# Kernel tuning notes

Hardware: AMD Instinct MI355X
Metric: run time of the kernel (lower is better)

Reference implementation:

```python
import jax, jax.numpy as jnp
import numpy as np


def causal_conv1d(x, w, b, dilation):
    # x: [B, Cin, S], w: [Cout, Cin, K] -> [B, Cout, S]
    # left pad by dilation*(K-1): equivalent to pad-both-sides + Chomp1d
    pad = dilation * (w.shape[-1] - 1)
    out = jax.lax.conv_general_dilated(
        x, w, window_strides=(1,), padding=[(pad, 0)],
        rhs_dilation=(dilation,), dimension_numbers=('NCH', 'OIH', 'NCH'))
    return out + b[None, :, None]


def temporal_block(x, w1, b1, w2, b2, dilation, ds=None):
    # dropout is identity in eval mode
    out = jax.nn.elu(causal_conv1d(x, w1, b1, dilation))
    out = jax.nn.elu(causal_conv1d(out, w2, b2, dilation))
    if ds is None:
        res = x
    else:
        ds_w, ds_b = ds
        res = causal_conv1d(x, ds_w, ds_b, 1)  # 1x1 downsample conv
    return jax.nn.elu(out + res)


def setup_inputs() -> dict:
    key = jax.random.key(0)
    ks = jax.random.split(key, 12)
    B, Cin, S, C, K, L = 16, 64, 4096, 128, 2, 5
    return {
        'x': jax.random.normal(ks[0], (B, Cin, S), jnp.float32),
        'w1_0': jax.random.normal(ks[1], (C, Cin, K), jnp.float32),
        'b1_0': jax.random.normal(ks[2], (C,), jnp.float32),
        'w2_0': jax.random.normal(ks[3], (C, C, K), jnp.float32),
        'b2_0': jax.random.normal(ks[4], (C,), jnp.float32),
        'ds_w': jax.random.normal(ks[5], (C, Cin, 1), jnp.float32),
        'ds_b': jax.random.normal(ks[6], (C,), jnp.float32),
        'W1': jax.random.normal(ks[7], (L - 1, C, C, K), jnp.float32),
        'B1': jax.random.normal(ks[8], (L - 1, C), jnp.float32),
        'W2': jax.random.normal(ks[9], (L - 1, C, C, K), jnp.float32),
        'B2': jax.random.normal(ks[10], (L - 1, C), jnp.float32),
    }


def reference(x, w1_0, b1_0, w2_0, b2_0, ds_w, ds_b, W1, B1, W2, B2):
    STEP = 3
    num_levels = 1 + W1.shape[0]  # 5
    outputs = [x]
    # layer 0: dilation 1, with downsample (64 -> 128 channels)
    x = temporal_block(x, w1_0, b1_0, w2_0, b2_0, 1, ds=(ds_w, ds_b))
    outputs.append(x)
    # layers 1..L-1: dilation 2**i, no downsample (128 -> 128)
    for i in range(1, num_levels):
        x = temporal_block(x, W1[i - 1], B1[i - 1], W2[i - 1], B2[i - 1], 2 ** i)
        outputs.append(x)
        if i >= STEP and outputs[i - STEP].shape == x.shape:
            x = x + outputs[i - STEP]
    return x
```

## Files before the change

kernel.cpp:

```cpp
#include <hip/hip_runtime.h>
#include <hip/hip_bf16.h>
#include <math.h>


typedef __attribute__((ext_vector_type(8))) short short8;
typedef __attribute__((ext_vector_type(4))) short short4v;
typedef __attribute__((ext_vector_type(4))) float floatx4;

#define S_LEN 4096
#define ROWS 192
#define AREG (ROWS * 128)
#define WBUF (128 * 128)
#define LDS_BYTES ((2 * AREG + 2 * WBUF) * 2)

#define OFF_DS     0
#define OFF_L0C1_0 8192
#define OFF_L0C1_1 16384
#define OFF_L0C2_0 24576
#define OFF_L0C2_1 40960
#define OFF_C1B    57344
#define OFF_C2B    188416

__device__ __forceinline__ float elu_f(float v) {
    return v > 0.0f ? v : (__expf(v) - 1.0f);
}
__device__ __forceinline__ short f2bs(float v) {
    __hip_bfloat16 h = __float2bfloat16(v);
    return *reinterpret_cast<short*>(&h);
}
__device__ __forceinline__ float bs2f(short s) {
    __hip_bfloat16 h = *reinterpret_cast<__hip_bfloat16*>(&s);
    return __bfloat162float(h);
}
__device__ __forceinline__ short4v pack4(const floatx4 v) {
    __hip_bfloat162 p0 = __float22bfloat162_rn(make_float2(v[0], v[1]));
    __hip_bfloat162 p1 = __float22bfloat162_rn(make_float2(v[2], v[3]));
    short4v r;
    r[0] = ((const short*)&p0)[0]; r[1] = ((const short*)&p0)[1];
    r[2] = ((const short*)&p1)[0]; r[3] = ((const short*)&p1)[1];
    return r;
}

__device__ __forceinline__ void gld_lds16(const void* g, void* l) {
    __builtin_amdgcn_global_load_lds(
        (const __attribute__((address_space(1))) void*)g,
        (__attribute__((address_space(3))) void*)l, 16, 0, 0);
}

template<int NSH>
__device__ __forceinline__ void stage_async(short* __restrict__ lds,
                                            const short* __restrict__ src,
                                            int wave, int lane)
{
    constexpr int NI = (NSH * 2) / 16384;
    const char* g = (const char*)src + wave * 1024 + lane * 16;
    char* l = (char*)lds + wave * 1024;
    #pragma unroll
    for (int i = 0; i < NI; ++i)
        gld_lds16(g + i * 16384, l + i * 16384);
}

__device__ __forceinline__ void mkoff(int (&o)[3], int srow, int l16, int quad, int d) {
    #pragma unroll
    for (int nt = 0; nt < 3; ++nt) {
        int r = srow + nt * 16 + l16 - d;
        if (r < 0) r = 0;
        o[nt] = (r >> 4) * 2048 + (r & 15) * 8 + quad * 128;
    }
}

template<int KCH>
__device__ __forceinline__ void conv_tap(const short* __restrict__ Lin,
                                         const short* __restrict__ Lw,
                                         const int (&ao)[3], floatx4 (&acc)[2][3])
{
    short8 wf[2][KCH];
    #pragma unroll
    for (int mt = 0; mt < 2; ++mt)
        #pragma unroll
        for (int kc = 0; kc < KCH; ++kc)
            wf[mt][kc] = *(const short8*)(Lw + mt * (KCH * 512) + kc * 512);
    #pragma unroll
    for (int nt = 0; nt < 3; ++nt) {
        const short* ab = Lin + ao[nt];
        #pragma unroll
        for (int kc = 0; kc < KCH; ++kc) {
            const short8 bf = *(const short8*)(ab + kc * 512);
            #pragma unroll
            for (int mt = 0; mt < 2; ++mt)
                acc[mt][nt] = __builtin_amdgcn_mfma_f32_16x16x32_bf16(wf[mt][kc], bf, acc[mt][nt], 0, 0, 0);
        }
    }
}

__device__ __forceinline__ void zero_acc(floatx4 (&acc)[2][3]) {
    #pragma unroll
    for (int mt = 0; mt < 2; ++mt)
        #pragma unroll
        for (int nt = 0; nt < 3; ++nt) acc[mt][nt] = {0.f, 0.f, 0.f, 0.f};
}

__global__ __launch_bounds__(1024, 4)
void tcn_fused(const float* __restrict__ x,
               const short* __restrict__ wq,
               const float* __restrict__ b1_0, const float* __restrict__ b2_0,
               const float* __restrict__ ds_b, const float* __restrict__ B1,
               const float* __restrict__ B2, float* __restrict__ out)
{
    extern __shared__ short L[];
    short* RA = L;
    short* RB = L + AREG;
    short* W0 = L + 2 * AREG;
    short* W1 = L + 2 * AREG + WBUF;

    const int tid  = threadIdx.x;
    const int wave = tid >> 6, lane = tid & 63;
    const int l16  = lane & 15, quad = lane >> 4;
    const int cobase = (wave & 3) * 32;
    const int srow   = (wave >> 2) * 48;
    const int s0  = blockIdx.x * 128;
    const int s0g = s0 - 64;
    const int b   = blockIdx.y;
    const bool zb = (s0 == 0);

    const int wqb2 = (cobase >> 4) * 1024 + quad * 128 + l16 * 8;
    const int wqb4 = (cobase >> 4) * 2048 + quad * 128 + l16 * 8;
    int aoff0[3], aoffd[3];
    mkoff(aoff0, srow, l16, quad, 0);
    int sb[3];
    #pragma unroll
    for (int nt = 0; nt < 3; ++nt) {
        const int sl = srow + nt * 16 + l16;
        sb[nt] = (sl >> 4) * 2048 + (sl & 15) * 8;
    }
    int ct[2];
    #pragma unroll
    for (int mt = 0; mt < 2; ++mt) {
        const int co4 = cobase + mt * 16 + quad * 4;
        ct[mt] = (co4 >> 5) * 512 + ((co4 >> 3) & 3) * 128 + (co4 & 7);
    }
    bool zr[3];
    #pragma unroll
    for (int nt = 0; nt < 3; ++nt) zr[nt] = zb && (srow + nt * 16 < 64);

    floatx4 acc[2][3];
    short4v x1keep[6];
    short4v dk[6];

    stage_async<8192>(W0, wq + OFF_DS, wave, lane);
    {
        const float* xp = x + (size_t)b * 64 * S_LEN;
        const int ci0 = wave * 4;
        const int cterm = (ci0 >> 5) * 512 + ((ci0 >> 3) & 3) * 128 + (ci0 & 7);
        #pragma unroll
        for (int h = 0; h < 3; ++h) {
            const int r = lane + h * 64;
            const int s = s0g + r;
            short4v pk;
            #pragma unroll
            for (int c4 = 0; c4 < 4; ++c4) {
                const float v = (s >= 0) ? xp[(ci0 + c4) * S_LEN + s] : 0.f;
                pk[c4] = f2bs(v);
            }
            *(short4v*)(RA + (r >> 4) * 2048 + (r & 15) * 8 + cterm) = pk;
        }
    }
    __syncthreads();

    stage_async<8192>(W1, wq + OFF_L0C1_0, wave, lane);
    zero_acc(acc);
    conv_tap<2>(RA, W0 + wqb2, aoff0, acc);
    #pragma unroll
    for (int mt = 0; mt < 2; ++mt) {
        const int co4 = cobase + mt * 16 + quad * 4;
        const floatx4 bb = *(const floatx4*)(ds_b + co4);
        #pragma unroll
        for (int nt = 0; nt < 3; ++nt) {
            floatx4 y = acc[mt][nt] + bb;
            if (zr[nt]) y = {0.f, 0.f, 0.f, 0.f};
            dk[mt * 3 + nt] = pack4(y);
        }
    }
    __syncthreads();

    stage_async<8192>(W0, wq + OFF_L0C1_1, wave, lane);
    mkoff(aoffd, srow, l16, quad, 1);
    zero_acc(acc);
    conv_tap<2>(RA, W1 + wqb2, aoffd, acc);
    __syncthreads();

    stage_async<16384>(W1, wq + OFF_L0C2_0, wave, lane);
    conv_tap<2>(RA, W0 + wqb2, aoff0, acc);
    #pragma unroll
    for (int mt = 0; mt < 2; ++mt) {
        const int co4 = cobase + mt * 16 + quad * 4;
        const floatx4 bb = *(const floatx4*)(b1_0 + co4);
        #pragma unroll
        for (int nt = 0; nt < 3; ++nt) {
            floatx4 y = acc[mt][nt] + bb;
            #pragma unroll
            for (int rr = 0; rr < 4; ++rr) y[rr] = elu_f(y[rr]);
            if (zr[nt]) y = {0.f, 0.f, 0.f, 0.f};
            *(short4v*)(RB + sb[nt] + ct[mt]) = pack4(y);
        }
    }
    __syncthreads();

    stage_async<16384>(W0, wq + OFF_L0C2_1, wave, lane);
    zero_acc(acc);
    conv_tap<4>(RB, W1 + wqb4, aoffd, acc);
    __syncthreads();

    stage_async<16384>(W1, wq + OFF_C1B, wave, lane);
    conv_tap<4>(RB, W0 + wqb4, aoff0, acc);
    #pragma unroll
    for (int mt = 0; mt < 2; ++mt) {
        const int co4 = cobase + mt * 16 + quad * 4;
        const floatx4 bb = *(const floatx4*)(b2_0 + co4);
        #pragma unroll
        for (int nt = 0; nt < 3; ++nt) {
            floatx4 y = acc[mt][nt] + bb;
            const short4v d4 = dk[mt * 3 + nt];
            #pragma unroll
            for (int rr = 0; rr < 4; ++rr) {
                y[rr] = elu_f(y[rr]);
                y[rr] = elu_f(y[rr] + bs2f(d4[rr]));
            }
            if (zr[nt]) y = {0.f, 0.f, 0.f, 0.f};
            const short4v pk = pack4(y);
            *(short4v*)(RA + sb[nt] + ct[mt]) = pk;
            x1keep[mt * 3 + nt] = pk;
        }
    }
    __syncthreads();

    #pragma unroll
    for (int lvl = 0; lvl < 3; ++lvl) {
        const int d = 2 << lvl;
        mkoff(aoffd, srow, l16, quad, d);
        stage_async<16384>(W0, wq + OFF_C1B + lvl * 32768 + 16384, wave, lane);
        zero_acc(acc);
        conv_tap<4>(RA, W1 + wqb4, aoffd, acc);
        __syncthreads();
        stage_async<16384>(W1, wq + OFF_C2B + lvl * 32768, wave, lane);
        conv_tap<4>(RA, W0 + wqb4, aoff0, acc);
        #pragma unroll
        for (int mt = 0; mt < 2; ++mt) {
            const int co4 = cobase + mt * 16 + quad * 4;
            const floatx4 bb = *(const floatx4*)(B1 + lvl * 128 + co4);
            #pragma unroll
            for (int nt = 0; nt < 3; ++nt) {
                floatx4 y = acc[mt][nt] + bb;
                #pragma unroll
                for (int rr = 0; rr < 4; ++rr) y[rr] = elu_f(y[rr]);
                if (zr[nt]) y = {0.f, 0.f, 0.f, 0.f};
                *(short4v*)(RB + sb[nt] + ct[mt]) = pack4(y);
            }
        }
        __syncthreads();
        stage_async<16384>(W0, wq + OFF_C2B + lvl * 32768 + 16384, wave, lane);
        zero_acc(acc);
        conv_tap<4>(RB, W1 + wqb4, aoffd, acc);
        __syncthreads();
        stage_async<16384>(W1, wq + OFF_C1B + (lvl + 1) * 32768, wave, lane);
        conv_tap<4>(RB, W0 + wqb4, aoff0, acc);
        #pragma unroll
        for (int mt = 0; mt < 2; ++mt) {
            const int co4 = cobase + mt * 16 + quad * 4;
            const floatx4 bb = *(const floatx4*)(B2 + lvl * 128 + co4);
            #pragma unroll
            for (int nt = 0; nt < 3; ++nt) {
                short* p = RA + sb[nt] + ct[mt];
                const short4v old = *(const short4v*)p;
                floatx4 y = acc[mt][nt] + bb;
                #pragma unroll
                for (int rr = 0; rr < 4; ++rr) {
                    y[rr] = elu_f(y[rr]);
                    y[rr] = elu_f(y[rr] + bs2f(old[rr]));
                }
                if (zr[nt]) y = {0.f, 0.f, 0.f, 0.f};
                *(short4v*)p = pack4(y);
            }
        }
        __syncthreads();
    }

    mkoff(aoffd, srow, l16, quad, 16);
    stage_async<16384>(W0, wq + OFF_C1B + 3 * 32768 + 16384, wave, lane);
    zero_acc(acc);
    conv_tap<4>(RA, W1 + wqb4, aoffd, acc);
    __syncthreads();
    stage_async<16384>(W1, wq + OFF_C2B + 3 * 32768, wave, lane);
    conv_tap<4>(RA, W0 + wqb4, aoff0, acc);
    #pragma unroll
    for (int mt = 0; mt < 2; ++mt) {
        const int co4 = cobase + mt * 16 + quad * 4;
        const floatx4 bb = *(const floatx4*)(B1 + 384 + co4);
        #pragma unroll
        for (int nt = 0; nt < 3; ++nt) {
            floatx4 y = acc[mt][nt] + bb;
            #pragma unroll
            for (int rr = 0; rr < 4; ++rr) y[rr] = elu_f(y[rr]);
            if (zr[nt]) y = {0.f, 0.f, 0.f, 0.f};
            *(short4v*)(RB + sb[nt] + ct[mt]) = pack4(y);
        }
    }
    __syncthreads();
    stage_async<16384>(W0, wq + OFF_C2B + 3 * 32768 + 16384, wave, lane);
    zero_acc(acc);
    conv_tap<4>(RB, W1 + wqb4, aoffd, acc);
    __syncthreads();
    conv_tap<4>(RB, W0 + wqb4, aoff0, acc);
    #pragma unroll
    for (int mt = 0; mt < 2; ++mt) {
        const int co4 = cobase + mt * 16 + quad * 4;
        const floatx4 bb = *(const floatx4*)(B2 + 384 + co4);
        #pragma unroll
        for (int nt = 0; nt < 3; ++nt) {
            if (srow + nt * 16 < 64) continue;
            const int sl = srow + nt * 16 + l16;
            const int sg = s0g + sl;
            const short4v res = *(const short4v*)(RA + sb[nt] + ct[mt]);
            const short4v k   = x1keep[mt * 3 + nt];
            #pragma unroll
            for (int rr = 0; rr < 4; ++rr) {
                float y = elu_f(acc[mt][nt][rr] + bb[rr]);
                y = elu_f(y + bs2f(res[rr]));
                y += bs2f(k[rr]);
                out[((size_t)(b * 128 + co4 + rr)) * S_LEN + sg] = y;
            }
        }
    }
}

__device__ __forceinline__ int widx(int co, int ci, int KC) {
    return (co >> 4) * (KC * 512) + (ci >> 5) * 512 + ((ci >> 3) & 3) * 128
         + (co & 15) * 8 + (ci & 7);
}

__global__ __launch_bounds__(256)
void prep_w(const float* __restrict__ w1_0, const float* __restrict__ w2_0,
            const float* __restrict__ ds_w, const float* __restrict__ W1,
            const float* __restrict__ W2, short* __restrict__ wq)
{
    int idx = blockIdx.x * 256 + threadIdx.x;
    const int n_c1 = 128 * 64;
    const int n_c2 = 128 * 128;
    if (idx < n_c1) {
        const int co = idx >> 6, ci = idx & 63;
        const int d = widx(co, ci, 2);
        wq[OFF_L0C1_0 + d] = f2bs(w1_0[idx * 2]);
        wq[OFF_L0C1_1 + d] = f2bs(w1_0[idx * 2 + 1]);
        return;
    }
    idx -= n_c1;
    if (idx < n_c2) {
        const int co = idx >> 7, ci = idx & 127;
        const int d = widx(co, ci, 4);
        wq[OFF_L0C2_0 + d] = f2bs(w2_0[idx * 2]);
        wq[OFF_L0C2_1 + d] = f2bs(w2_0[idx * 2 + 1]);
        return;
    }
    idx -= n_c2;
    if (idx < 4 * n_c2) {
        const int li = idx / n_c2, j = idx - li * n_c2;
        const int co = j >> 7, ci = j & 127;
        const int d = widx(co, ci, 4);
        wq[OFF_C1B + li * 32768 + d]         = f2bs(W1[(li * n_c2 + j) * 2]);
        wq[OFF_C1B + li * 32768 + 16384 + d] = f2bs(W1[(li * n_c2 + j) * 2 + 1]);
        return;
    }
    idx -= 4 * n_c2;
    if (idx < 4 * n_c2) {
        const int li = idx / n_c2, j = idx - li * n_c2;
        const int co = j >> 7, ci = j & 127;
        const int d = widx(co, ci, 4);
        wq[OFF_C2B + li * 32768 + d]         = f2bs(W2[(li * n_c2 + j) * 2]);
        wq[OFF_C2B + li * 32768 + 16384 + d] = f2bs(W2[(li * n_c2 + j) * 2 + 1]);
        return;
    }
    idx -= 4 * n_c2;
    if (idx < n_c1) {
        const int co = idx >> 6, ci = idx & 63;
        wq[OFF_DS + widx(co, ci, 2)] = f2bs(ds_w[idx]);
    }
}

extern "C" void kernel_launch(void* const* d_in, const int* in_sizes, int n_in,
                              void* d_out, int out_size, void* d_ws, size_t ws_size,
                              hipStream_t stream) {
    const float* x_in = (const float*)d_in[0];
    const float* w1_0 = (const float*)d_in[1];
    const float* b1_0 = (const float*)d_in[2];
    const float* w2_0 = (const float*)d_in[3];
    const float* b2_0 = (const float*)d_in[4];
    const float* ds_w = (const float*)d_in[5];
    const float* ds_b = (const float*)d_in[6];
    const float* W1   = (const float*)d_in[7];
    const float* B1   = (const float*)d_in[8];
    const float* W2   = (const float*)d_in[9];
    const float* B2   = (const float*)d_in[10];
    float* out = (float*)d_out;

    short* wq = (short*)d_ws;

    (void)hipFuncSetAttribute((const void*)tcn_fused,
                              hipFuncAttributeMaxDynamicSharedMemorySize, LDS_BYTES);

    prep_w<<<dim3(640), 256, 0, stream>>>(w1_0, w2_0, ds_w, W1, W2, wq);
    tcn_fused<<<dim3(32, 16), dim3(1024), LDS_BYTES, stream>>>(
        x_in, wq, b1_0, b2_0, ds_b, B1, B2, out);
}
```

Measured before the change: 171.6 us.

## Skip dead halo rows per level, prefetch layer-0 weights, add MFMA priority

The fused TCN kernel now skips MFMA tiles and epilogues for halo rows whose outputs can no longer reach the final 128 output rows, based on a per-level minimum valid row (receptive-field shrinkage). It also stages two layer-0 weight buffers up front and swaps the W0/W1 ping-pong roles, which removes one barrier. It adds s_setprio around the MFMA loops and makes the wave index scalar via readfirstlane. Skipping leaves stale data in the skipped rows, so correctness depends on those rows never being read by rows that are still computed.

```diff
diff --git a/kernel.cpp b/kernel.cpp
--- a/kernel.cpp
+++ b/kernel.cpp
@@ -69,19 +69,27 @@
     }
 }
 
+__device__ __forceinline__ int ntfloor(int minrow, int srow) {
+    return (minrow > srow) ? ((minrow - srow + 15) >> 4) : 0;
+}
+
 template<int KCH>
 __device__ __forceinline__ void conv_tap(const short* __restrict__ Lin,
                                          const short* __restrict__ Lw,
-                                         const int (&ao)[3], floatx4 (&acc)[2][3])
+                                         const int (&ao)[3], floatx4 (&acc)[2][3],
+                                         const int nt0)
 {
+    if (nt0 >= 3) return;
     short8 wf[2][KCH];
     #pragma unroll
     for (int mt = 0; mt < 2; ++mt)
         #pragma unroll
         for (int kc = 0; kc < KCH; ++kc)
             wf[mt][kc] = *(const short8*)(Lw + mt * (KCH * 512) + kc * 512);
+    __builtin_amdgcn_s_setprio(1);
     #pragma unroll
     for (int nt = 0; nt < 3; ++nt) {
+        if (nt < nt0) continue;
         const short* ab = Lin + ao[nt];
         #pragma unroll
         for (int kc = 0; kc < KCH; ++kc) {
@@ -91,6 +99,7 @@
                 acc[mt][nt] = __builtin_amdgcn_mfma_f32_16x16x32_bf16(wf[mt][kc], bf, acc[mt][nt], 0, 0, 0);
         }
     }
+    __builtin_amdgcn_s_setprio(0);
 }
 
 __device__ __forceinline__ void zero_acc(floatx4 (&acc)[2][3]) {
@@ -114,7 +123,8 @@
     short* W1 = L + 2 * AREG + WBUF;
 
     const int tid  = threadIdx.x;
-    const int wave = tid >> 6, lane = tid & 63;
+    const int wave = __builtin_amdgcn_readfirstlane(tid >> 6);
+    const int lane = tid & 63;
     const int l16  = lane & 15, quad = lane >> 4;
     const int cobase = (wave & 3) * 32;
     const int srow   = (wave >> 2) * 48;
@@ -148,6 +158,7 @@
     short4v dk[6];
 
     stage_async<8192>(W0, wq + OFF_DS, wave, lane);
+    stage_async<8192>(W0 + 8192, wq + OFF_L0C1_0, wave, lane);
     {
         const float* xp = x + (size_t)b * 64 * S_LEN;
         const int ci0 = wave * 4;
@@ -167,9 +178,9 @@
     }
     __syncthreads();
 
-    stage_async<8192>(W1, wq + OFF_L0C1_0, wave, lane);
+    stage_async<8192>(W1, wq + OFF_L0C1_1, wave, lane);
     zero_acc(acc);
-    conv_tap<2>(RA, W0 + wqb2, aoff0, acc);
+    conv_tap<2>(RA, W0 + wqb2, aoff0, acc, 0);
     #pragma unroll
     for (int mt = 0; mt < 2; ++mt) {
         const int co4 = cobase + mt * 16 + quad * 4;
@@ -181,16 +192,13 @@
             dk[mt * 3 + nt] = pack4(y);
         }
     }
-    __syncthreads();
-
-    stage_async<8192>(W0, wq + OFF_L0C1_1, wave, lane);
     mkoff(aoffd, srow, l16, quad, 1);
     zero_acc(acc);
-    conv_tap<2>(RA, W1 + wqb2, aoffd, acc);
+    conv_tap<2>(RA, W0 + 8192 + wqb2, aoffd, acc, 0);
     __syncthreads();
 
-    stage_async<16384>(W1, wq + OFF_L0C2_0, wave, lane);
-    conv_tap<2>(RA, W0 + wqb2, aoff0, acc);
+    stage_async<16384>(W0, wq + OFF_L0C2_0, wave, lane);
+    conv_tap<2>(RA, W1 + wqb2, aoff0, acc, 0);
     #pragma unroll
     for (int mt = 0; mt < 2; ++mt) {
         const int co4 = cobase + mt * 16 + quad * 4;
@@ -206,13 +214,13 @@
     }
     __syncthreads();
 
-    stage_async<16384>(W0, wq + OFF_L0C2_1, wave, lane);
+    stage_async<16384>(W1, wq + OFF_L0C2_1, wave, lane);
     zero_acc(acc);
-    conv_tap<4>(RB, W1 + wqb4, aoffd, acc);
+    conv_tap<4>(RB, W0 + wqb4, aoffd, acc, 0);
     __syncthreads();
 
-    stage_async<16384>(W1, wq + OFF_C1B, wave, lane);
-    conv_tap<4>(RB, W0 + wqb4, aoff0, acc);
+    stage_async<16384>(W0, wq + OFF_C1B, wave, lane);
+    conv_tap<4>(RB, W1 + wqb4, aoff0, acc, 0);
     #pragma unroll
     for (int mt = 0; mt < 2; ++mt) {
         const int co4 = cobase + mt * 16 + quad * 4;
@@ -234,22 +242,27 @@
     }
     __syncthreads();
 
+    const int mc1[3] = {0, 0, 16};
+    const int mc2[3] = {0, 16, 32};
     #pragma unroll
     for (int lvl = 0; lvl < 3; ++lvl) {
         const int d = 2 << lvl;
+        const int n1 = ntfloor(mc1[lvl], srow);
+        const int n2 = ntfloor(mc2[lvl], srow);
         mkoff(aoffd, srow, l16, quad, d);
-        stage_async<16384>(W0, wq + OFF_C1B + lvl * 32768 + 16384, wave, lane);
+        stage_async<16384>(W1, wq + OFF_C1B + lvl * 32768 + 16384, wave, lane);
         zero_acc(acc);
-        conv_tap<4>(RA, W1 + wqb4, aoffd, acc);
-        __syncthreads();
-        stage_async<16384>(W1, wq + OFF_C2B + lvl * 32768, wave, lane);
-        conv_tap<4>(RA, W0 + wqb4, aoff0, acc);
+        conv_tap<4>(RA, W0 + wqb4, aoffd, acc, n1);
+        __syncthreads();
+        stage_async<16384>(W0, wq + OFF_C2B + lvl * 32768, wave, lane);
+        conv_tap<4>(RA, W1 + wqb4, aoff0, acc, n1);
         #pragma unroll
         for (int mt = 0; mt < 2; ++mt) {
             const int co4 = cobase + mt * 16 + quad * 4;
             const floatx4 bb = *(const floatx4*)(B1 + lvl * 128 + co4);
             #pragma unroll
             for (int nt = 0; nt < 3; ++nt) {
+                if (nt < n1) continue;
                 floatx4 y = acc[mt][nt] + bb;
                 #pragma unroll
                 for (int rr = 0; rr < 4; ++rr) y[rr] = elu_f(y[rr]);
@@ -258,18 +271,19 @@
             }
         }
         __syncthreads();
-        stage_async<16384>(W0, wq + OFF_C2B + lvl * 32768 + 16384, wave, lane);
+        stage_async<16384>(W1, wq + OFF_C2B + lvl * 32768 + 16384, wave, lane);
         zero_acc(acc);
-        conv_tap<4>(RB, W1 + wqb4, aoffd, acc);
-        __syncthreads();
-        stage_async<16384>(W1, wq + OFF_C1B + (lvl + 1) * 32768, wave, lane);
-        conv_tap<4>(RB, W0 + wqb4, aoff0, acc);
+        conv_tap<4>(RB, W0 + wqb4, aoffd, acc, n2);
+        __syncthreads();
+        stage_async<16384>(W0, wq + OFF_C1B + (lvl + 1) * 32768, wave, lane);
+        conv_tap<4>(RB, W1 + wqb4, aoff0, acc, n2);
         #pragma unroll
         for (int mt = 0; mt < 2; ++mt) {
             const int co4 = cobase + mt * 16 + quad * 4;
             const floatx4 bb = *(const floatx4*)(B2 + lvl * 128 + co4);
             #pragma unroll
             for (int nt = 0; nt < 3; ++nt) {
+                if (nt < n2) continue;
                 short* p = RA + sb[nt] + ct[mt];
                 const short4v old = *(const short4v*)p;
                 floatx4 y = acc[mt][nt] + bb;
@@ -285,49 +299,54 @@
         __syncthreads();
     }
 
-    mkoff(aoffd, srow, l16, quad, 16);
-    stage_async<16384>(W0, wq + OFF_C1B + 3 * 32768 + 16384, wave, lane);
-    zero_acc(acc);
-    conv_tap<4>(RA, W1 + wqb4, aoffd, acc);
-    __syncthreads();
-    stage_async<16384>(W1, wq + OFF_C2B + 3 * 32768, wave, lane);
-    conv_tap<4>(RA, W0 + wqb4, aoff0, acc);
-    #pragma unroll
-    for (int mt = 0; mt < 2; ++mt) {
-        const int co4 = cobase + mt * 16 + quad * 4;
-        const floatx4 bb = *(const floatx4*)(B1 + 384 + co4);
-        #pragma unroll
-        for (int nt = 0; nt < 3; ++nt) {
-            floatx4 y = acc[mt][nt] + bb;
-            #pragma unroll
-            for (int rr = 0; rr < 4; ++rr) y[rr] = elu_f(y[rr]);
-            if (zr[nt]) y = {0.f, 0.f, 0.f, 0.f};
-            *(short4v*)(RB + sb[nt] + ct[mt]) = pack4(y);
-        }
-    }
-    __syncthreads();
-    stage_async<16384>(W0, wq + OFF_C2B + 3 * 32768 + 16384, wave, lane);
-    zero_acc(acc);
-    conv_tap<4>(RB, W1 + wqb4, aoffd, acc);
-    __syncthreads();
-    conv_tap<4>(RB, W0 + wqb4, aoff0, acc);
-    #pragma unroll
-    for (int mt = 0; mt < 2; ++mt) {
-        const int co4 = cobase + mt * 16 + quad * 4;
-        const floatx4 bb = *(const floatx4*)(B2 + 384 + co4);
-        #pragma unroll
-        for (int nt = 0; nt < 3; ++nt) {
-            if (srow + nt * 16 < 64) continue;
-            const int sl = srow + nt * 16 + l16;
-            const int sg = s0g + sl;
-            const short4v res = *(const short4v*)(RA + sb[nt] + ct[mt]);
-            const short4v k   = x1keep[mt * 3 + nt];
-            #pragma unroll
-            for (int rr = 0; rr < 4; ++rr) {
-                float y = elu_f(acc[mt][nt][rr] + bb[rr]);
-                y = elu_f(y + bs2f(res[rr]));
-                y += bs2f(k[rr]);
-                out[((size_t)(b * 128 + co4 + rr)) * S_LEN + sg] = y;
+    {
+        const int n1 = ntfloor(48, srow);
+        const int n2 = ntfloor(64, srow);
+        mkoff(aoffd, srow, l16, quad, 16);
+        stage_async<16384>(W1, wq + OFF_C1B + 3 * 32768 + 16384, wave, lane);
+        zero_acc(acc);
+        conv_tap<4>(RA, W0 + wqb4, aoffd, acc, n1);
+        __syncthreads();
+        stage_async<16384>(W0, wq + OFF_C2B + 3 * 32768, wave, lane);
+        conv_tap<4>(RA, W1 + wqb4, aoff0, acc, n1);
+        #pragma unroll
+        for (int mt = 0; mt < 2; ++mt) {
+            const int co4 = cobase + mt * 16 + quad * 4;
+            const floatx4 bb = *(const floatx4*)(B1 + 384 + co4);
+            #pragma unroll
+            for (int nt = 0; nt < 3; ++nt) {
+                if (nt < n1) continue;
+                floatx4 y = acc[mt][nt] + bb;
+                #pragma unroll
+                for (int rr = 0; rr < 4; ++rr) y[rr] = elu_f(y[rr]);
+                if (zr[nt]) y = {0.f, 0.f, 0.f, 0.f};
+                *(short4v*)(RB + sb[nt] + ct[mt]) = pack4(y);
+            }
+        }
+        __syncthreads();
+        stage_async<16384>(W1, wq + OFF_C2B + 3 * 32768 + 16384, wave, lane);
+        zero_acc(acc);
+        conv_tap<4>(RB, W0 + wqb4, aoffd, acc, n2);
+        __syncthreads();
+        conv_tap<4>(RB, W1 + wqb4, aoff0, acc, n2);
+        #pragma unroll
+        for (int mt = 0; mt < 2; ++mt) {
+            const int co4 = cobase + mt * 16 + quad * 4;
+            const floatx4 bb = *(const floatx4*)(B2 + 384 + co4);
+            #pragma unroll
+            for (int nt = 0; nt < 3; ++nt) {
+                if (srow + nt * 16 < 64) continue;
+                const int sl = srow + nt * 16 + l16;
+                const int sg = s0g + sl;
+                const short4v res = *(const short4v*)(RA + sb[nt] + ct[mt]);
+                const short4v k   = x1keep[mt * 3 + nt];
+                #pragma unroll
+                for (int rr = 0; rr < 4; ++rr) {
+                    float y = elu_f(acc[mt][nt][rr] + bb[rr]);
+                    y = elu_f(y + bs2f(res[rr]));
+                    y += bs2f(k[rr]);
+                    out[((size_t)(b * 128 + co4 + rr)) * S_LEN + sg] = y;
+                }
             }
         }
     }
```

Result: no change. 168.6 us (-1.7%).
